# Performance work log

Hardware: AMD Instinct MI355X
Metric: run time of the kernel (lower is better)

## Reference

```python
import jax, jax.numpy as jnp
import numpy as np

N_NODES = 20000; N_EDGES = 200000
FN = 128; FE = 64; D = 128; T = 128; K = 5
H = 4; DH = D // H; N_LAYERS = 2; FF = 4 * D
B = 32768
T0 = 0.0; EPS = 1e-5


def _ln(x, s, b):
    m = jnp.mean(x, axis=-1, keepdims=True)
    v = jnp.mean(jnp.square(x - m), axis=-1, keepdims=True)
    return (x - m) / jnp.sqrt(v + EPS) * s + b


def setup_inputs() -> dict:
    key = jax.random.key(0)
    ks = jax.random.split(key, 24)
    def w(i, shape, s=0.05):
        return jax.random.normal(ks[i], shape, jnp.float32) * s
    return {
        "src": jax.random.randint(ks[0], (B,), 0, N_NODES),
        "dst": jax.random.randint(ks[1], (B,), 0, N_NODES),
        "neg": jax.random.randint(ks[2], (B,), 0, N_NODES),
        "eidx": jax.random.randint(ks[3], (B,), 0, N_EDGES),
        "ts": jax.random.uniform(ks[4], (B,), jnp.float32) * 1000.0,
        "node_feats": w(5, (N_NODES, FN), 1.0),
        "edge_feats": w(6, (N_EDGES, FE), 1.0),
        "node_lin_w": w(7, (D, FN)), "node_lin_b": jnp.zeros((D,), jnp.float32),
        "edge_lin_w": w(8, (D, FE)), "edge_lin_b": jnp.zeros((D,), jnp.float32),
        "time_w": w(9, (T,), 1.0), "time_b": w(10, (T,), 1.0),
        "tok_w": w(11, (D, 3 * D + T)), "tok_b": jnp.zeros((D,), jnp.float32),
        "qkv_w": w(12, (N_LAYERS, 3 * D, D)), "qkv_b": jnp.zeros((N_LAYERS, 3 * D), jnp.float32),
        "attn_w": w(13, (N_LAYERS, D, D)), "attn_b": jnp.zeros((N_LAYERS, D), jnp.float32),
        "ln1_s": jnp.ones((N_LAYERS, D), jnp.float32), "ln1_b": jnp.zeros((N_LAYERS, D), jnp.float32),
        "ln2_s": jnp.ones((N_LAYERS, D), jnp.float32), "ln2_b": jnp.zeros((N_LAYERS, D), jnp.float32),
        "ff1_w": w(14, (N_LAYERS, FF, D)), "ff1_b": jnp.zeros((N_LAYERS, FF), jnp.float32),
        "ff2_w": w(15, (N_LAYERS, D, FF)), "ff2_b": jnp.zeros((N_LAYERS, D), jnp.float32),
        "p1_w": w(16, (D, D)), "p1_b": jnp.zeros((D,), jnp.float32),
        "p2_w": w(17, (K, D)), "p2_b": jnp.zeros((K,), jnp.float32),
    }


def reference(src, dst, neg, eidx, ts, node_feats, edge_feats,
              node_lin_w, node_lin_b, edge_lin_w, edge_lin_b,
              time_w, time_b, tok_w, tok_b,
              qkv_w, qkv_b, attn_w, attn_b,
              ln1_s, ln1_b, ln2_s, ln2_b,
              ff1_w, ff1_b, ff2_w, ff2_b,
              p1_w, p1_b, p2_w, p2_b):
    # --- occurrence tokens: [src occs | dst occs | neg occs] = 3B tokens ---
    self_nodes = jnp.concatenate([src, dst, neg])          # [3B]
    other_nodes = jnp.concatenate([dst, src, src])         # [3B]
    eidx_all = jnp.concatenate([eidx, eidx, eidx])
    ts_all = jnp.concatenate([ts, ts, ts])
    Ntot = self_nodes.shape[0]

    base_self = node_feats[self_nodes] @ node_lin_w.T + node_lin_b    # [3B, D]
    base_other = node_feats[other_nodes] @ node_lin_w.T + node_lin_b
    edge_emb = edge_feats[eidx_all] @ edge_lin_w.T + edge_lin_b       # [3B, D]
    time_emb = jnp.cos((ts_all - T0)[:, None] * time_w[None, :] + time_b)  # [3B, T]
    x_cat = jnp.concatenate([base_self, base_other, edge_emb, time_emb], axis=-1)
    tok = jax.nn.relu(x_cat @ tok_w.T + tok_b)                        # [3B, D]

    # --- group occurrences by node, sort by time, pad (device-side) ---
    node_ids = jnp.unique(self_nodes)                      # [Nn]
    order = jnp.lexsort((ts_all, self_nodes))              # primary node, secondary time
    nodes_s = self_nodes[order]
    row_s = jnp.searchsorted(node_ids, nodes_s)            # row per sorted occ
    starts = jnp.searchsorted(nodes_s, node_ids)           # start of each group
    pos_s = jnp.arange(Ntot) - starts[row_s]               # pos within group
    node_row = jnp.zeros((Ntot,), jnp.int32).at[order].set(row_s.astype(jnp.int32))
    pos_map = jnp.zeros((Ntot,), jnp.int32).at[order].set(pos_s.astype(jnp.int32))
    seq_len = jnp.diff(jnp.concatenate([starts, jnp.array([Ntot], starts.dtype)]))
    Nn = int(node_ids.shape[0])
    Lmax = int(seq_len.max())

    x_pad = jnp.zeros((Nn, Lmax, D), tok.dtype).at[node_row, pos_map].set(tok)
    pad_mask = jnp.arange(Lmax)[None, :] >= seq_len[:, None]  # True = padded key

    # --- pre-LN TransformerEncoder (gelu, no final norm) ---
    scale = jnp.float32(1.0 / np.sqrt(DH))
    x = x_pad
    for l in range(N_LAYERS):
        h = _ln(x, ln1_s[l], ln1_b[l])
        qkv = h @ qkv_w[l].T + qkv_b[l]                    # [Nn, L, 3D]
        q, k, v = jnp.split(qkv, 3, axis=-1)
        q = q.reshape(Nn, Lmax, H, DH); k = k.reshape(Nn, Lmax, H, DH); v = v.reshape(Nn, Lmax, H, DH)
        scores = jnp.einsum('nqhd,nkhd->nhqk', q, k) * scale
        scores = jnp.where(pad_mask[:, None, None, :], jnp.float32(-1e9), scores)
        a = jax.nn.softmax(scores, axis=-1)
        o = jnp.einsum('nhqk,nkhd->nqhd', a, v).reshape(Nn, Lmax, D)
        x = x + o @ attn_w[l].T + attn_b[l]
        h2 = _ln(x, ln2_s[l], ln2_b[l])
        x = x + jax.nn.gelu(h2 @ ff1_w[l].T + ff1_b[l], approximate=False) @ ff2_w[l].T + ff2_b[l]

    # --- gather per-occurrence outputs and project to community probs ---
    def proj(hh):
        return jax.nn.softmax(jax.nn.relu(hh @ p1_w.T + p1_b) @ p2_w.T + p2_b, axis=-1)
    src_h = x[node_row[:B], pos_map[:B]]
    dst_h = x[node_row[B:2 * B], pos_map[B:2 * B]]
    neg_h = x[node_row[2 * B:], pos_map[2 * B:]]
    return proj(src_h), proj(dst_h), proj(neg_h)
```

## Files before the change

### kernel.cpp

```cpp
#include <hip/hip_runtime.h>
#include <hip/hip_bf16.h>
#include <math.h>

#define NB 32768
#define NTOK (3 * NB)
#define NNODES 20000
#define MAXL 64

typedef short bf16x8 __attribute__((ext_vector_type(8)));
typedef float f32x4 __attribute__((ext_vector_type(4)));

typedef __attribute__((address_space(3))) void lds_t;
typedef const __attribute__((address_space(1))) void gbl_t;

__device__ __forceinline__ float b2f(short s) {
    unsigned int u = ((unsigned int)(unsigned short)s) << 16;
    union { unsigned int u; float f; } c;
    c.u = u;
    return c.f;
}


__global__ void convert_k(const float* __restrict__ in, __hip_bfloat16* __restrict__ out, int n) {
    int i = blockIdx.x * 256 + threadIdx.x;
    int stride = gridDim.x * 256;
    for (; i < n; i += stride) out[i] = __float2bfloat16(in[i]);
}

__global__ void fold12_k(const float* __restrict__ tok_w, const float* __restrict__ nl_w,
                         __hip_bfloat16* __restrict__ A12) {
    int idx = blockIdx.x * 256 + threadIdx.x;
    if (idx >= 256 * 128) return;
    int n = idx >> 7, f = idx & 127;
    const float* tw = (n < 128) ? (tok_w + n * 512) : (tok_w + (n - 128) * 512 + 128);
    float acc = 0.f;
    for (int c = 0; c < 128; ++c) acc += tw[c] * nl_w[c * 128 + f];
    A12[idx] = __float2bfloat16(acc);
}

__global__ void foldE_k(const float* __restrict__ tok_w, const float* __restrict__ el_w,
                        __hip_bfloat16* __restrict__ AE) {
    int idx = blockIdx.x * 256 + threadIdx.x;
    if (idx >= 128 * 192) return;
    int d = idx / 192, j = idx % 192;
    float acc;
    if (j < 64) {
        acc = 0.f;
        for (int c = 0; c < 128; ++c) acc += tok_w[d * 512 + 256 + c] * el_w[c * 64 + j];
    } else {
        acc = tok_w[d * 512 + 384 + (j - 64)];
    }
    AE[idx] = __float2bfloat16(acc);
}

__global__ void foldb_k(const float* __restrict__ tok_w, const float* __restrict__ tok_b,
                        const float* __restrict__ nl_b, const float* __restrict__ el_b,
                        float* __restrict__ bf) {
    int d = threadIdx.x;
    if (d >= 128) return;
    float acc = tok_b[d];
    for (int c = 0; c < 128; ++c)
        acc += (tok_w[d * 512 + c] + tok_w[d * 512 + 128 + c]) * nl_b[c];
    for (int c = 0; c < 128; ++c)
        acc += tok_w[d * 512 + 256 + c] * el_b[c];
    bf[d] = acc;
}

__device__ __forceinline__ int self_node(int t, const int* src, const int* dst, const int* neg) {
    if (t < NB) return src[t];
    if (t < 2 * NB) return dst[t - NB];
    return neg[t - 2 * NB];
}

__global__ void count_k(const int* __restrict__ src, const int* __restrict__ dst,
                        const int* __restrict__ neg, int* __restrict__ cnt) {
    int t = blockIdx.x * 256 + threadIdx.x;
    if (t >= NTOK) return;
    atomicAdd(&cnt[self_node(t, src, dst, neg)], 1);
}

__global__ __launch_bounds__(1024) void scan_k(const int* __restrict__ cnt,
                                               int* __restrict__ starts) {
    __shared__ int ps[1024];
    int t = threadIdx.x;
    const int PER = 20;
    int base = t * PER;
    int loc[PER];
    int s = 0;
#pragma unroll
    for (int k = 0; k < PER; ++k) {
        int i = base + k;
        int v = (i < NNODES) ? cnt[i] : 0;
        loc[k] = s;
        s += v;
    }
    ps[t] = s;
    __syncthreads();
    for (int off = 1; off < 1024; off <<= 1) {
        int v = (t >= off) ? ps[t - off] : 0;
        __syncthreads();
        ps[t] += v;
        __syncthreads();
    }
    int offv = (t > 0) ? ps[t - 1] : 0;
#pragma unroll
    for (int k = 0; k < PER; ++k) {
        int i = base + k;
        if (i < NNODES) starts[i] = offv + loc[k];
    }
}

__global__ void scatter_k(const int* __restrict__ src, const int* __restrict__ dst,
                          const int* __restrict__ neg, const int* __restrict__ starts,
                          int* __restrict__ cursor, int* __restrict__ order) {
    int t = blockIdx.x * 256 + threadIdx.x;
    if (t >= NTOK) return;
    int node = self_node(t, src, dst, neg);
    int p = atomicAdd(&cursor[node], 1);
    order[starts[node] + p] = t;
}

__global__ void aemb_k(const int* __restrict__ eidx, const float* __restrict__ ts,
                       const float* __restrict__ ef, const float* __restrict__ tw,
                       const float* __restrict__ tb, __hip_bfloat16* __restrict__ Aemb) {
    int idx = blockIdx.x * 256 + threadIdx.x;
    if (idx >= NB * 192) return;
    int m = idx / 192, j = idx % 192;
    float v;
    if (j < 64) v = ef[(size_t)eidx[m] * 64 + j];
    else { int c = j - 64; v = cosf(ts[m] * tw[c] + tb[c]); }
    Aemb[idx] = __float2bfloat16(v);
}

__global__ __launch_bounds__(256) void asm_emb_k(
    const int* __restrict__ order, const int* __restrict__ src, const int* __restrict__ dst,
    const int* __restrict__ neg, const float* __restrict__ P12, const float* __restrict__ E,
    const float* __restrict__ s, const float* __restrict__ b,
    float* __restrict__ x, __hip_bfloat16* __restrict__ h) {
    int p = blockIdx.x * 4 + (threadIdx.x >> 6);
    int lane = threadIdx.x & 63;
    int t = order[p];
    int m, self, other;
    if (t < NB) { m = t; self = src[m]; other = dst[m]; }
    else if (t < 2 * NB) { m = t - NB; self = dst[m]; other = src[m]; }
    else { m = t - 2 * NB; self = neg[m]; other = src[m]; }
    int d0 = lane, d1 = lane + 64;
    float v0 = P12[(size_t)self * 256 + d0] + P12[(size_t)other * 256 + 128 + d0] +
               E[(size_t)m * 128 + d0];
    float v1 = P12[(size_t)self * 256 + d1] + P12[(size_t)other * 256 + 128 + d1] +
               E[(size_t)m * 128 + d1];
    v0 = fmaxf(v0, 0.f);
    v1 = fmaxf(v1, 0.f);
    float sum = v0 + v1;
#pragma unroll
    for (int off = 32; off; off >>= 1) sum += __shfl_xor(sum, off, 64);
    float mean = sum * (1.f / 128.f);
    float c0 = v0 - mean, c1 = v1 - mean;
    float vs = c0 * c0 + c1 * c1;
#pragma unroll
    for (int off = 32; off; off >>= 1) vs += __shfl_xor(vs, off, 64);
    float inv = rsqrtf(vs * (1.f / 128.f) + 1e-5f);
    x[(size_t)p * 128 + d0] = v0;
    x[(size_t)p * 128 + d1] = v1;
    h[(size_t)p * 128 + d0] = __float2bfloat16(c0 * inv * s[d0] + b[d0]);
    h[(size_t)p * 128 + d1] = __float2bfloat16(c1 * inv * s[d1] + b[d1]);
}

__device__ __forceinline__ float gelu_f(float v) {
    float ax = fabsf(v) * 0.70710678118654752f;
    float t = 1.f / (1.f + 0.3275911f * ax);
    float poly = ((((1.061405429f * t - 1.453152027f) * t + 1.421413741f) * t -
                   0.284496736f) * t + 0.254829592f) * t;
    float erf_ax = 1.f - poly * __expf(-ax * ax);
    float erfv = (v < 0.f) ? -erf_ax : erf_ax;
    return 0.5f * v * (1.f + erfv);
}

#define G_F32 0
#define G_BF16 1
#define G_GELU 2
#define G_ADD_LN 3
#define G_ADD_BF16 4

template <int MODE>
__global__ __launch_bounds__(256, 4) void gemm5_k(
    const __hip_bfloat16* __restrict__ A, const __hip_bfloat16* __restrict__ B,
    const float* __restrict__ bias, float* __restrict__ x,
    const float* __restrict__ lns, const float* __restrict__ lnb,
    __hip_bfloat16* __restrict__ hout, float* __restrict__ Cf, int N, int K) {
    __shared__ __align__(16) __hip_bfloat16 sA[2][128 * 32];
    __shared__ __align__(16) __hip_bfloat16 sB[2][128 * 32];
    __shared__ float redS[2][128];
    __shared__ float redS2[2][128];
    int tid = threadIdx.x;
    int lane = tid & 63, wid = tid >> 6;
    int wm = wid & 1, wn = wid >> 1;
    int mBase = blockIdx.x * 128, nBase = blockIdx.y * 128;
    f32x4 acc[4][4];
#pragma unroll
    for (int i = 0; i < 4; ++i)
#pragma unroll
        for (int j = 0; j < 4; ++j) {
            f32x4 z = {0.f, 0.f, 0.f, 0.f};
            acc[i][j] = z;
        }

    auto stage = [&](int buf, int k0) {
#pragma unroll
        for (int i = 0; i < 2; ++i) {
            int cid = i * 256 + tid;
            int row = cid >> 2, slotS = cid & 3;
            int slotG = slotS ^ (row & 3);
            const __hip_bfloat16* ga = A + (size_t)(mBase + row) * K + k0 + slotG * 8;
            const __hip_bfloat16* gb = B + (size_t)(nBase + row) * K + k0 + slotG * 8;
            __builtin_amdgcn_global_load_lds((gbl_t*)ga, (lds_t*)&sA[buf][(cid & ~63) * 8],
                                             16, 0, 0);
            __builtin_amdgcn_global_load_lds((gbl_t*)gb, (lds_t*)&sB[buf][(cid & ~63) * 8],
                                             16, 0, 0);
        }
    };

    int nt = K >> 5;
    stage(0, 0);
    int cur = 0;
    for (int t = 0; t < nt; ++t) {
        if (t + 1 < nt) {
            stage(cur ^ 1, (t + 1) << 5);
            asm volatile("s_waitcnt vmcnt(4)" ::: "memory");
        } else {
            asm volatile("s_waitcnt vmcnt(0)" ::: "memory");
        }
        __builtin_amdgcn_s_barrier();
        __builtin_amdgcn_sched_barrier(0);
        const bf16x8* AsV = reinterpret_cast<const bf16x8*>(sA[cur]);
        const bf16x8* BsV = reinterpret_cast<const bf16x8*>(sB[cur]);
        bf16x8 a[4], b[4];
        int kvec = lane >> 4;
#pragma unroll
        for (int f = 0; f < 4; ++f) {
            int ra = wm * 64 + f * 16 + (lane & 15);
            a[f] = AsV[ra * 4 + (kvec ^ (ra & 3))];
            int rb = wn * 64 + f * 16 + (lane & 15);
            b[f] = BsV[rb * 4 + (kvec ^ (rb & 3))];
        }
        __builtin_amdgcn_s_setprio(1);
#pragma unroll
        for (int fm = 0; fm < 4; ++fm)
#pragma unroll
            for (int fn = 0; fn < 4; ++fn)
                acc[fm][fn] = __builtin_amdgcn_mfma_f32_16x16x32_bf16(
                    a[fm], b[fn], acc[fm][fn], 0, 0, 0);
        __builtin_amdgcn_s_setprio(0);
        __builtin_amdgcn_s_barrier();
        cur ^= 1;
    }

    if (MODE == G_F32 || MODE == G_BF16 || MODE == G_GELU) {
        int colBase = nBase + wn * 64;
#pragma unroll
        for (int fm = 0; fm < 4; ++fm) {
            int row0 = mBase + wm * 64 + fm * 16 + (lane >> 4) * 4;
#pragma unroll
            for (int fn = 0; fn < 4; ++fn) {
                int col = colBase + fn * 16 + (lane & 15);
                float bv = bias ? bias[col] : 0.f;
#pragma unroll
                for (int j = 0; j < 4; ++j) {
                    float v = acc[fm][fn][j] + bv;
                    if (MODE == G_F32) {
                        Cf[(size_t)(row0 + j) * N + col] = v;
                    } else if (MODE == G_GELU) {
                        hout[(size_t)(row0 + j) * N + col] = __float2bfloat16(gelu_f(v));
                    } else {
                        hout[(size_t)(row0 + j) * N + col] = __float2bfloat16(v);
                    }
                }
            }
        }
    } else {
#pragma unroll
        for (int fm = 0; fm < 4; ++fm) {
            int rl0 = wm * 64 + fm * 16 + (lane >> 4) * 4;
#pragma unroll
            for (int fn = 0; fn < 4; ++fn) {
                int col = wn * 64 + fn * 16 + (lane & 15);
                float bv = bias[col];
#pragma unroll
                for (int j = 0; j < 4; ++j) {
                    size_t off = (size_t)(mBase + rl0 + j) * 128 + col;
                    float v = acc[fm][fn][j] + bv + x[off];
                    x[off] = v;
                    acc[fm][fn][j] = v;
                }
            }
        }
        if (MODE == G_ADD_BF16) {
#pragma unroll
            for (int fm = 0; fm < 4; ++fm) {
                int rl0 = wm * 64 + fm * 16 + (lane >> 4) * 4;
#pragma unroll
                for (int fn = 0; fn < 4; ++fn) {
                    int col = wn * 64 + fn * 16 + (lane & 15);
#pragma unroll
                    for (int j = 0; j < 4; ++j)
                        hout[(size_t)(mBase + rl0 + j) * 128 + col] =
                            __float2bfloat16(acc[fm][fn][j]);
                }
            }
        } else {
#pragma unroll
            for (int fm = 0; fm < 4; ++fm) {
#pragma unroll
                for (int j = 0; j < 4; ++j) {
                    float s1 = 0.f, s2 = 0.f;
#pragma unroll
                    for (int fn = 0; fn < 4; ++fn) {
                        float v = acc[fm][fn][j];
                        s1 += v;
                        s2 += v * v;
                    }
#pragma unroll
                    for (int off = 1; off < 16; off <<= 1) {
                        s1 += __shfl_xor(s1, off, 64);
                        s2 += __shfl_xor(s2, off, 64);
                    }
                    if ((lane & 15) == 0) {
                        int rl = wm * 64 + fm * 16 + (lane >> 4) * 4 + j;
                        redS[wn][rl] = s1;
                        redS2[wn][rl] = s2;
                    }
                }
            }
            __syncthreads();
#pragma unroll
            for (int fm = 0; fm < 4; ++fm) {
                int rl0 = wm * 64 + fm * 16 + (lane >> 4) * 4;
#pragma unroll
                for (int j = 0; j < 4; ++j) {
                    int rl = rl0 + j;
                    float mean = (redS[0][rl] + redS[1][rl]) * (1.f / 128.f);
                    float var = (redS2[0][rl] + redS2[1][rl]) * (1.f / 128.f) - mean * mean;
                    float inv = rsqrtf(var + 1e-5f);
#pragma unroll
                    for (int fn = 0; fn < 4; ++fn) {
                        int col = wn * 64 + fn * 16 + (lane & 15);
                        float c = (acc[fm][fn][j] - mean) * inv;
                        hout[(size_t)(mBase + rl) * 128 + col] =
                            __float2bfloat16(c * lns[col] + lnb[col]);
                    }
                }
            }
        }
    }
}

__global__ __launch_bounds__(256) void attn_k(
    const __hip_bfloat16* __restrict__ qkv, const int* __restrict__ starts,
    const int* __restrict__ cnt, __hip_bfloat16* __restrict__ o) {
    __shared__ float sc[4][4][4][MAXL];
    int wid = threadIdx.x >> 6, lane = threadIdx.x & 63;
    int node = blockIdx.x * 4 + wid;
    if (node >= NNODES) return;
    int st = starts[node];
    int len = cnt[node];
    if (len <= 0) return;
    if (len > MAXL) len = MAXL;
    int qs = lane >> 4, li = lane & 15, h = li >> 2;
    const float scale = 0.17677669529663687f;

    for (int qb = 0; qb < len; qb += 4) {
        int qi = qb + qs;
        bool act = qi < len;
        int qidx = act ? qi : len - 1;
        bf16x8 qv = *reinterpret_cast<const bf16x8*>(
            qkv + (size_t)(st + qidx) * 384 + li * 8);
        float qf[8];
#pragma unroll
        for (int e = 0; e < 8; ++e) qf[e] = b2f(qv[e]);
        for (int j = 0; j < len; ++j) {
            bf16x8 kv = *reinterpret_cast<const bf16x8*>(
                qkv + (size_t)(st + j) * 384 + 128 + li * 8);
            float d = 0.f;
#pragma unroll
            for (int e = 0; e < 8; ++e) d += qf[e] * b2f(kv[e]);
            d += __shfl_xor(d, 1, 64);
            d += __shfl_xor(d, 2, 64);
            if ((li & 3) == 0) sc[wid][qs][h][j] = d * scale;
        }
        float mx = -1e30f;
        for (int j = li & 3; j < len; j += 4) mx = fmaxf(mx, sc[wid][qs][h][j]);
        mx = fmaxf(mx, __shfl_xor(mx, 1, 64));
        mx = fmaxf(mx, __shfl_xor(mx, 2, 64));
        float ssum = 0.f;
        for (int j = li & 3; j < len; j += 4) {
            float e = __expf(sc[wid][qs][h][j] - mx);
            sc[wid][qs][h][j] = e;
            ssum += e;
        }
        ssum += __shfl_xor(ssum, 1, 64);
        ssum += __shfl_xor(ssum, 2, 64);
        float sinv = 1.f / ssum;
        float accv[8] = {0.f, 0.f, 0.f, 0.f, 0.f, 0.f, 0.f, 0.f};
        for (int j = 0; j < len; ++j) {
            float p = sc[wid][qs][h][j];
            bf16x8 vv = *reinterpret_cast<const bf16x8*>(
                qkv + (size_t)(st + j) * 384 + 256 + li * 8);
#pragma unroll
            for (int e = 0; e < 8; ++e) accv[e] += p * b2f(vv[e]);
        }
        if (act) {
            bf16x8 ov;
#pragma unroll
            for (int e = 0; e < 8; ++e) {
                __hip_bfloat16 t = __float2bfloat16(accv[e] * sinv);
                ov[e] = *reinterpret_cast<short*>(&t);
            }
            *reinterpret_cast<bf16x8*>(o + (size_t)(st + qi) * 128 + li * 8) = ov;
        }
    }
}

__global__ __launch_bounds__(256) void p1head_k(
    const __hip_bfloat16* __restrict__ A, const __hip_bfloat16* __restrict__ B,
    const float* __restrict__ bias, const float* __restrict__ p2w,
    const float* __restrict__ p2b, const int* __restrict__ order,
    float* __restrict__ out) {
    __shared__ __align__(16) char smem[65536];
    __shared__ float p2s[640];
    __shared__ float p2bs[5];
    float4* As4 = (float4*)smem;
    float4* Bs4 = (float4*)(smem + 16384);
    float* rowbuf = (float*)smem;
    int tid = threadIdx.x;
    for (int i = tid; i < 640; i += 256) p2s[i] = p2w[i];
    if (tid < 5) p2bs[tid] = p2b[tid];
    int lane = tid & 63, wid = tid >> 6;
    int wm = wid & 1, wn = wid >> 1;
    int mBase = blockIdx.x * 128;
    f32x4 acc[4][4];
#pragma unroll
    for (int i = 0; i < 4; ++i)
#pragma unroll
        for (int j = 0; j < 4; ++j) {
            f32x4 z = {0.f, 0.f, 0.f, 0.f};
            acc[i][j] = z;
        }
    bf16x8* AsV = reinterpret_cast<bf16x8*>(As4);
    bf16x8* BsV = reinterpret_cast<bf16x8*>(Bs4);
    for (int k0 = 0; k0 < 128; k0 += 64) {
#pragma unroll
        for (int i = 0; i < 4; ++i) {
            int cid = i * 256 + tid;
            int r = cid >> 3, c = cid & 7;
            int sidx = r * 8 + (c ^ (r & 7));
            As4[sidx] = *reinterpret_cast<const float4*>(A + (size_t)(mBase + r) * 128 + k0 + c * 8);
            Bs4[sidx] = *reinterpret_cast<const float4*>(B + (size_t)r * 128 + k0 + c * 8);
        }
        __syncthreads();
#pragma unroll
        for (int kk = 0; kk < 2; ++kk) {
            bf16x8 a[4], bb[4];
            int ccol = kk * 4 + (lane >> 4);
#pragma unroll
            for (int f = 0; f < 4; ++f) {
                int ra = wm * 64 + f * 16 + (lane & 15);
                a[f] = AsV[ra * 8 + (ccol ^ (ra & 7))];
                int rb = wn * 64 + f * 16 + (lane & 15);
                bb[f] = BsV[rb * 8 + (ccol ^ (rb & 7))];
            }
#pragma unroll
            for (int fm = 0; fm < 4; ++fm)
#pragma unroll
                for (int fn = 0; fn < 4; ++fn)
                    acc[fm][fn] = __builtin_amdgcn_mfma_f32_16x16x32_bf16(
                        a[fm], bb[fn], acc[fm][fn], 0, 0, 0);
        }
        __syncthreads();
    }
#pragma unroll
    for (int fm = 0; fm < 4; ++fm) {
        int rl0 = wm * 64 + fm * 16 + (lane >> 4) * 4;
#pragma unroll
        for (int fn = 0; fn < 4; ++fn) {
            int col = wn * 64 + fn * 16 + (lane & 15);
            float bv = bias[col];
#pragma unroll
            for (int j = 0; j < 4; ++j) {
                int rl = rl0 + j;
                rowbuf[rl * 128 + (col ^ ((rl & 7) << 2))] = fmaxf(acc[fm][fn][j] + bv, 0.f);
            }
        }
    }
    __syncthreads();
    int row = tid >> 1, half = tid & 1;
    int swz = (row & 7) << 2;
    float lg[5] = {0.f, 0.f, 0.f, 0.f, 0.f};
    for (int i = 0; i < 64; ++i) {
        int col = half * 64 + i;
        float rv = rowbuf[row * 128 + (col ^ swz)];
#pragma unroll
        for (int k = 0; k < 5; ++k) lg[k] += rv * p2s[k * 128 + col];
    }
#pragma unroll
    for (int k = 0; k < 5; ++k) lg[k] += __shfl_xor(lg[k], 1, 64);
    if (half == 0) {
        float mx = -1e30f;
#pragma unroll
        for (int k = 0; k < 5; ++k) {
            lg[k] += p2bs[k];
            mx = fmaxf(mx, lg[k]);
        }
        float e[5], ssum = 0.f;
#pragma unroll
        for (int k = 0; k < 5; ++k) {
            e[k] = __expf(lg[k] - mx);
            ssum += e[k];
        }
        float si = 1.f / ssum;
        int t = order[mBase + row];
#pragma unroll
        for (int k = 0; k < 5; ++k) out[(size_t)t * 5 + k] = e[k] * si;
    }
}


extern "C" void kernel_launch(void* const* d_in, const int* in_sizes, int n_in,
                              void* d_out, int out_size, void* d_ws, size_t ws_size,
                              hipStream_t stream) {
    const int* src = (const int*)d_in[0];
    const int* dst = (const int*)d_in[1];
    const int* neg = (const int*)d_in[2];
    const int* eidx = (const int*)d_in[3];
    const float* ts = (const float*)d_in[4];
    const float* node_feats = (const float*)d_in[5];
    const float* edge_feats = (const float*)d_in[6];
    const float* node_lin_w = (const float*)d_in[7];
    const float* node_lin_b = (const float*)d_in[8];
    const float* edge_lin_w = (const float*)d_in[9];
    const float* edge_lin_b = (const float*)d_in[10];
    const float* time_w = (const float*)d_in[11];
    const float* time_b = (const float*)d_in[12];
    const float* tok_w = (const float*)d_in[13];
    const float* tok_b = (const float*)d_in[14];
    const float* qkv_w = (const float*)d_in[15];
    const float* qkv_b = (const float*)d_in[16];
    const float* attn_w = (const float*)d_in[17];
    const float* attn_b = (const float*)d_in[18];
    const float* ln1_s = (const float*)d_in[19];
    const float* ln1_b = (const float*)d_in[20];
    const float* ln2_s = (const float*)d_in[21];
    const float* ln2_b = (const float*)d_in[22];
    const float* ff1_w = (const float*)d_in[23];
    const float* ff1_b = (const float*)d_in[24];
    const float* ff2_w = (const float*)d_in[25];
    const float* ff2_b = (const float*)d_in[26];
    const float* p1_w = (const float*)d_in[27];
    const float* p1_b = (const float*)d_in[28];
    const float* p2_w = (const float*)d_in[29];
    const float* p2_b = (const float*)d_in[30];
    float* out = (float*)d_out;

    char* w = (char*)d_ws;
    auto alloc = [&](size_t bytes) {
        char* p = w;
        w += (bytes + 255) & ~(size_t)255;
        return p;
    };
    float* x = (float*)alloc((size_t)NTOK * 128 * 4);
    __hip_bfloat16* h = (__hip_bfloat16*)alloc((size_t)NTOK * 128 * 2);
    char* big = alloc((size_t)(NTOK + 64) * 512 * 2);
    __hip_bfloat16* qkvb = (__hip_bfloat16*)big;
    __hip_bfloat16* ob = (__hip_bfloat16*)(big + (size_t)(NTOK + 64) * 384 * 2);
    __hip_bfloat16* ub = (__hip_bfloat16*)big;
    float* P12 = (float*)alloc((size_t)(NNODES + 96) * 256 * 4);
    float* E = (float*)alloc((size_t)NB * 128 * 4);
    __hip_bfloat16* Aemb = (__hip_bfloat16*)alloc((size_t)NB * 192 * 2);
    __hip_bfloat16* nfb = (__hip_bfloat16*)alloc((size_t)(NNODES + 96) * 128 * 2);
    __hip_bfloat16* A12 = (__hip_bfloat16*)alloc(256 * 128 * 2);
    __hip_bfloat16* AE = (__hip_bfloat16*)alloc(128 * 192 * 2);
    float* bfold = (float*)alloc(128 * 4);
    __hip_bfloat16* qkvwb = (__hip_bfloat16*)alloc(2 * 384 * 128 * 2);
    __hip_bfloat16* attnwb = (__hip_bfloat16*)alloc(2 * 128 * 128 * 2);
    __hip_bfloat16* ff1wb = (__hip_bfloat16*)alloc(2 * 512 * 128 * 2);
    __hip_bfloat16* ff2wb = (__hip_bfloat16*)alloc(2 * 128 * 512 * 2);
    __hip_bfloat16* p1wb = (__hip_bfloat16*)alloc(128 * 128 * 2);
    int* cnt = (int*)alloc(NNODES * 4);
    int* starts = (int*)alloc(NNODES * 4);
    int* cursor = (int*)alloc(NNODES * 4);
    int* order = (int*)alloc(NTOK * 4);

    hipMemsetAsync(cnt, 0, NNODES * 4, stream);
    hipMemsetAsync(cursor, 0, NNODES * 4, stream);

    auto cvt = [&](const float* in, __hip_bfloat16* outp, int n) {
        int blocks = (n + 255) / 256;
        if (blocks > 2048) blocks = 2048;
        convert_k<<<blocks, 256, 0, stream>>>(in, outp, n);
    };
    cvt(node_feats, nfb, NNODES * 128);
    cvt(qkv_w, qkvwb, 2 * 384 * 128);
    cvt(attn_w, attnwb, 2 * 128 * 128);
    cvt(ff1_w, ff1wb, 2 * 512 * 128);
    cvt(ff2_w, ff2wb, 2 * 128 * 512);
    cvt(p1_w, p1wb, 128 * 128);

    fold12_k<<<128, 256, 0, stream>>>(tok_w, node_lin_w, A12);
    foldE_k<<<96, 256, 0, stream>>>(tok_w, edge_lin_w, AE);
    foldb_k<<<1, 128, 0, stream>>>(tok_w, tok_b, node_lin_b, edge_lin_b, bfold);

    count_k<<<(NTOK + 255) / 256, 256, 0, stream>>>(src, dst, neg, cnt);
    scan_k<<<1, 1024, 0, stream>>>(cnt, starts);
    scatter_k<<<(NTOK + 255) / 256, 256, 0, stream>>>(src, dst, neg, starts, cursor, order);

    aemb_k<<<(NB * 192 + 255) / 256, 256, 0, stream>>>(eidx, ts, edge_feats, time_w, time_b, Aemb);

    gemm5_k<G_F32><<<dim3(157, 2), 256, 0, stream>>>(
        nfb, A12, nullptr, nullptr, nullptr, nullptr, nullptr, P12, 256, 128);
    gemm5_k<G_F32><<<dim3(256, 1), 256, 0, stream>>>(
        Aemb, AE, bfold, nullptr, nullptr, nullptr, nullptr, E, 128, 192);
    asm_emb_k<<<NTOK / 4, 256, 0, stream>>>(order, src, dst, neg, P12, E,
                                            ln1_s, ln1_b, x, h);

    const int gm = NTOK / 128;
    for (int l = 0; l < 2; ++l) {
        gemm5_k<G_BF16><<<dim3(gm, 3), 256, 0, stream>>>(
            h, qkvwb + (size_t)l * 384 * 128, qkv_b + l * 384,
            nullptr, nullptr, nullptr, qkvb, nullptr, 384, 128);
        attn_k<<<(NNODES + 3) / 4, 256, 0, stream>>>(qkvb, starts, cnt, ob);
        gemm5_k<G_ADD_LN><<<dim3(gm, 1), 256, 0, stream>>>(
            ob, attnwb + (size_t)l * 128 * 128, attn_b + l * 128,
            x, ln2_s + l * 128, ln2_b + l * 128, h, nullptr, 128, 128);
        gemm5_k<G_GELU><<<dim3(gm, 4), 256, 0, stream>>>(
            h, ff1wb + (size_t)l * 512 * 128, ff1_b + l * 512,
            nullptr, nullptr, nullptr, ub, nullptr, 512, 128);
        if (l == 0)
            gemm5_k<G_ADD_LN><<<dim3(gm, 1), 256, 0, stream>>>(
                ub, ff2wb, ff2_b, x, ln1_s + 128, ln1_b + 128, h, nullptr, 128, 512);
        else
            gemm5_k<G_ADD_BF16><<<dim3(gm, 1), 256, 0, stream>>>(
                ub, ff2wb + (size_t)128 * 512, ff2_b + 128, x,
                nullptr, nullptr, h, nullptr, 128, 512);
    }

    p1head_k<<<gm, 256, 0, stream>>>(h, p1wb, p1_b, p2_w, p2_b, order, out);
}
```

Measured before the change: 604.1 us.

## Add weight-resident persistent GEMM kernel with vectorized epilogues for K≤192 GEMMs

Adds gemm6_k, which loads the full 128-column weight tile for the whole K dimension into LDS once. It then loops persistently over M tiles, double-buffering only the activation tile and prefetching the next tile's first chunk. The MFMA operands are swapped so each lane holds 4 consecutive columns, which allows float4 and bf16x4 vector stores and float4 bias and LN-parameter loads in the epilogue. The LDS swizzle in gemm5_k is strengthened to reduce bank conflicts. The trade-off is more LDS per block (lower occupancy, launch bounds 3) and fixed persistent grid sizes in exchange for removing repeated weight reloads and scalar stores.

```diff
diff --git a/kernel.cpp b/kernel.cpp
--- a/kernel.cpp
+++ b/kernel.cpp
@@ -8,6 +8,7 @@
 #define MAXL 64
 
 typedef short bf16x8 __attribute__((ext_vector_type(8)));
+typedef short bf16x4 __attribute__((ext_vector_type(4)));
 typedef float f32x4 __attribute__((ext_vector_type(4)));
 
 typedef __attribute__((address_space(3))) void lds_t;
@@ -18,6 +19,16 @@
     union { unsigned int u; float f; } c;
     c.u = u;
     return c.f;
+}
+
+__device__ __forceinline__ void store4(__hip_bfloat16* p, float a, float b, float c, float d) {
+    bf16x4 o;
+    __hip_bfloat16 t;
+    t = __float2bfloat16(a); o[0] = *reinterpret_cast<short*>(&t);
+    t = __float2bfloat16(b); o[1] = *reinterpret_cast<short*>(&t);
+    t = __float2bfloat16(c); o[2] = *reinterpret_cast<short*>(&t);
+    t = __float2bfloat16(d); o[3] = *reinterpret_cast<short*>(&t);
+    *reinterpret_cast<bf16x4*>(p) = o;
 }
 
 
@@ -182,6 +193,179 @@
 #define G_ADD_LN 3
 #define G_ADD_BF16 4
 
+template <int MODE, int KK>
+__global__ __launch_bounds__(256, 3) void gemm6_k(
+    const __hip_bfloat16* __restrict__ A, const __hip_bfloat16* __restrict__ B,
+    const float* __restrict__ bias, float* __restrict__ x,
+    const float* __restrict__ lns, const float* __restrict__ lnb,
+    __hip_bfloat16* __restrict__ hout, float* __restrict__ Cf,
+    int N, int numM) {
+    constexpr int CH = KK / 32;
+    constexpr int BSLOT = KK / 8;
+    __shared__ __align__(16) __hip_bfloat16 sB[128 * KK];
+    __shared__ __align__(16) __hip_bfloat16 sA[2][128 * 32];
+    int tid = threadIdx.x;
+    int lane = tid & 63, wid = tid >> 6;
+    int li = lane & 15, lq = lane >> 4;
+    int nBase = blockIdx.y * 128;
+
+#pragma unroll
+    for (int i = 0; i < KK / 16; ++i) {
+        int cid = i * 256 + tid;
+        int row = cid / BSLOT, slotS = cid % BSLOT;
+        int slotG = slotS ^ (row & 7);
+        const __hip_bfloat16* gb = B + (size_t)(nBase + row) * KK + slotG * 8;
+        __builtin_amdgcn_global_load_lds((gbl_t*)gb, (lds_t*)&sB[(cid & ~63) * 8], 16, 0, 0);
+    }
+    auto stageA = [&](int buf, int mi, int c) {
+#pragma unroll
+        for (int i = 0; i < 2; ++i) {
+            int cid = i * 256 + tid;
+            int row = cid >> 2, slotS = cid & 3;
+            int slotG = slotS ^ ((row & 3) ^ ((row >> 2) & 3));
+            const __hip_bfloat16* ga =
+                A + (size_t)(mi * 128 + row) * KK + c * 32 + slotG * 8;
+            __builtin_amdgcn_global_load_lds((gbl_t*)ga, (lds_t*)&sA[buf][(cid & ~63) * 8],
+                                             16, 0, 0);
+        }
+    };
+
+    int mi = blockIdx.x;
+    if (mi < numM) stageA(0, mi, 0);
+    const bf16x8* BsV = reinterpret_cast<const bf16x8*>(sB);
+
+    while (mi < numM) {
+        int nextMi = mi + gridDim.x;
+        f32x4 acc[2][8];
+#pragma unroll
+        for (int i = 0; i < 2; ++i)
+#pragma unroll
+            for (int j = 0; j < 8; ++j) {
+                f32x4 z = {0.f, 0.f, 0.f, 0.f};
+                acc[i][j] = z;
+            }
+        for (int c = 0; c < CH; ++c) {
+            if (c + 1 < CH) {
+                stageA((c + 1) & 1, mi, c + 1);
+                asm volatile("s_waitcnt vmcnt(2)" ::: "memory");
+            } else if (nextMi < numM) {
+                stageA(0, nextMi, 0);
+                asm volatile("s_waitcnt vmcnt(2)" ::: "memory");
+            } else {
+                asm volatile("s_waitcnt vmcnt(0)" ::: "memory");
+            }
+            __builtin_amdgcn_s_barrier();
+            __builtin_amdgcn_sched_barrier(0);
+            const bf16x8* AsV = reinterpret_cast<const bf16x8*>(sA[c & 1]);
+            bf16x8 a[2], b[8];
+#pragma unroll
+            for (int fm = 0; fm < 2; ++fm) {
+                int ra = wid * 32 + fm * 16 + li;
+                a[fm] = AsV[ra * 4 + (lq ^ ((ra & 3) ^ ((ra >> 2) & 3)))];
+            }
+            int kvb = c * 4 + lq;
+#pragma unroll
+            for (int fn = 0; fn < 8; ++fn) {
+                int rb = fn * 16 + li;
+                b[fn] = BsV[rb * BSLOT + (kvb ^ (rb & 7))];
+            }
+            __builtin_amdgcn_s_setprio(1);
+#pragma unroll
+            for (int fm = 0; fm < 2; ++fm)
+#pragma unroll
+                for (int fn = 0; fn < 8; ++fn)
+                    acc[fm][fn] = __builtin_amdgcn_mfma_f32_16x16x32_bf16(
+                        b[fn], a[fm], acc[fm][fn], 0, 0, 0);
+            __builtin_amdgcn_s_setprio(0);
+            __builtin_amdgcn_s_barrier();
+        }
+        int rowG0 = mi * 128 + wid * 32;
+        if (MODE == G_F32 || MODE == G_BF16 || MODE == G_GELU) {
+#pragma unroll
+            for (int fm = 0; fm < 2; ++fm) {
+                int row = rowG0 + fm * 16 + li;
+#pragma unroll
+                for (int fn = 0; fn < 8; ++fn) {
+                    int col = nBase + fn * 16 + lq * 4;
+                    float4 bv = {0.f, 0.f, 0.f, 0.f};
+                    if (bias) bv = *reinterpret_cast<const float4*>(bias + col);
+                    f32x4 v = acc[fm][fn];
+                    float v0 = v[0] + bv.x, v1 = v[1] + bv.y;
+                    float v2 = v[2] + bv.z, v3 = v[3] + bv.w;
+                    if (MODE == G_GELU) {
+                        v0 = gelu_f(v0); v1 = gelu_f(v1); v2 = gelu_f(v2); v3 = gelu_f(v3);
+                    }
+                    if (MODE == G_F32) {
+                        float4 o = {v0, v1, v2, v3};
+                        *reinterpret_cast<float4*>(Cf + (size_t)row * N + col) = o;
+                    } else {
+                        store4(hout + (size_t)row * N + col, v0, v1, v2, v3);
+                    }
+                }
+            }
+        } else {
+            float s1[2] = {0.f, 0.f}, s2[2] = {0.f, 0.f};
+#pragma unroll
+            for (int fm = 0; fm < 2; ++fm) {
+                int row = rowG0 + fm * 16 + li;
+#pragma unroll
+                for (int fn = 0; fn < 8; ++fn) {
+                    int col = fn * 16 + lq * 4;
+                    float4 bv = *reinterpret_cast<const float4*>(bias + col);
+                    float4 xv = *reinterpret_cast<float4*>(x + (size_t)row * 128 + col);
+                    f32x4 v = acc[fm][fn];
+                    v[0] += bv.x + xv.x; v[1] += bv.y + xv.y;
+                    v[2] += bv.z + xv.z; v[3] += bv.w + xv.w;
+                    acc[fm][fn] = v;
+                    float4 o = {v[0], v[1], v[2], v[3]};
+                    *reinterpret_cast<float4*>(x + (size_t)row * 128 + col) = o;
+                    s1[fm] += v[0] + v[1] + v[2] + v[3];
+                    s2[fm] += v[0] * v[0] + v[1] * v[1] + v[2] * v[2] + v[3] * v[3];
+                }
+            }
+            if (MODE == G_ADD_BF16) {
+#pragma unroll
+                for (int fm = 0; fm < 2; ++fm) {
+                    int row = rowG0 + fm * 16 + li;
+#pragma unroll
+                    for (int fn = 0; fn < 8; ++fn) {
+                        int col = fn * 16 + lq * 4;
+                        f32x4 v = acc[fm][fn];
+                        store4(hout + (size_t)row * 128 + col, v[0], v[1], v[2], v[3]);
+                    }
+                }
+            } else {
+#pragma unroll
+                for (int fm = 0; fm < 2; ++fm) {
+                    float a1 = s1[fm];
+                    a1 += __shfl_xor(a1, 16, 64);
+                    a1 += __shfl_xor(a1, 32, 64);
+                    float a2 = s2[fm];
+                    a2 += __shfl_xor(a2, 16, 64);
+                    a2 += __shfl_xor(a2, 32, 64);
+                    float mean = a1 * (1.f / 128.f);
+                    float var = a2 * (1.f / 128.f) - mean * mean;
+                    float inv = rsqrtf(var + 1e-5f);
+                    int row = rowG0 + fm * 16 + li;
+#pragma unroll
+                    for (int fn = 0; fn < 8; ++fn) {
+                        int col = fn * 16 + lq * 4;
+                        float4 sv = *reinterpret_cast<const float4*>(lns + col);
+                        float4 bv2 = *reinterpret_cast<const float4*>(lnb + col);
+                        f32x4 v = acc[fm][fn];
+                        store4(hout + (size_t)row * 128 + col,
+                               (v[0] - mean) * inv * sv.x + bv2.x,
+                               (v[1] - mean) * inv * sv.y + bv2.y,
+                               (v[2] - mean) * inv * sv.z + bv2.z,
+                               (v[3] - mean) * inv * sv.w + bv2.w);
+                    }
+                }
+            }
+        }
+        mi = nextMi;
+    }
+}
+
 template <int MODE>
 __global__ __launch_bounds__(256, 4) void gemm5_k(
     const __hip_bfloat16* __restrict__ A, const __hip_bfloat16* __restrict__ B,
@@ -210,7 +394,7 @@
         for (int i = 0; i < 2; ++i) {
             int cid = i * 256 + tid;
             int row = cid >> 2, slotS = cid & 3;
-            int slotG = slotS ^ (row & 3);
+            int slotG = slotS ^ ((row & 3) ^ ((row >> 2) & 3));
             const __hip_bfloat16* ga = A + (size_t)(mBase + row) * K + k0 + slotG * 8;
             const __hip_bfloat16* gb = B + (size_t)(nBase + row) * K + k0 + slotG * 8;
             __builtin_amdgcn_global_load_lds((gbl_t*)ga, (lds_t*)&sA[buf][(cid & ~63) * 8],
@@ -239,9 +423,9 @@
 #pragma unroll
         for (int f = 0; f < 4; ++f) {
             int ra = wm * 64 + f * 16 + (lane & 15);
-            a[f] = AsV[ra * 4 + (kvec ^ (ra & 3))];
+            a[f] = AsV[ra * 4 + (kvec ^ ((ra & 3) ^ ((ra >> 2) & 3)))];
             int rb = wn * 64 + f * 16 + (lane & 15);
-            b[f] = BsV[rb * 4 + (kvec ^ (rb & 3))];
+            b[f] = BsV[rb * 4 + (kvec ^ ((rb & 3) ^ ((rb >> 2) & 3)))];
         }
         __builtin_amdgcn_s_setprio(1);
 #pragma unroll
@@ -255,99 +439,75 @@
         cur ^= 1;
     }
 
-    if (MODE == G_F32 || MODE == G_BF16 || MODE == G_GELU) {
-        int colBase = nBase + wn * 64;
-#pragma unroll
-        for (int fm = 0; fm < 4; ++fm) {
-            int row0 = mBase + wm * 64 + fm * 16 + (lane >> 4) * 4;
-#pragma unroll
-            for (int fn = 0; fn < 4; ++fn) {
-                int col = colBase + fn * 16 + (lane & 15);
-                float bv = bias ? bias[col] : 0.f;
-#pragma unroll
-                for (int j = 0; j < 4; ++j) {
-                    float v = acc[fm][fn][j] + bv;
-                    if (MODE == G_F32) {
-                        Cf[(size_t)(row0 + j) * N + col] = v;
-                    } else if (MODE == G_GELU) {
-                        hout[(size_t)(row0 + j) * N + col] = __float2bfloat16(gelu_f(v));
-                    } else {
-                        hout[(size_t)(row0 + j) * N + col] = __float2bfloat16(v);
-                    }
-                }
-            }
-        }
-    } else {
+#pragma unroll
+    for (int fm = 0; fm < 4; ++fm) {
+        int rl0 = wm * 64 + fm * 16 + (lane >> 4) * 4;
+#pragma unroll
+        for (int fn = 0; fn < 4; ++fn) {
+            int col = wn * 64 + fn * 16 + (lane & 15);
+            float bv = bias[col];
+#pragma unroll
+            for (int j = 0; j < 4; ++j) {
+                size_t off = (size_t)(mBase + rl0 + j) * 128 + col;
+                float v = acc[fm][fn][j] + bv + x[off];
+                x[off] = v;
+                acc[fm][fn][j] = v;
+            }
+        }
+    }
+    if (MODE == G_ADD_BF16) {
 #pragma unroll
         for (int fm = 0; fm < 4; ++fm) {
             int rl0 = wm * 64 + fm * 16 + (lane >> 4) * 4;
 #pragma unroll
             for (int fn = 0; fn < 4; ++fn) {
                 int col = wn * 64 + fn * 16 + (lane & 15);
-                float bv = bias[col];
-#pragma unroll
-                for (int j = 0; j < 4; ++j) {
-                    size_t off = (size_t)(mBase + rl0 + j) * 128 + col;
-                    float v = acc[fm][fn][j] + bv + x[off];
-                    x[off] = v;
-                    acc[fm][fn][j] = v;
+#pragma unroll
+                for (int j = 0; j < 4; ++j)
+                    hout[(size_t)(mBase + rl0 + j) * 128 + col] =
+                        __float2bfloat16(acc[fm][fn][j]);
+            }
+        }
+    } else {
+#pragma unroll
+        for (int fm = 0; fm < 4; ++fm) {
+#pragma unroll
+            for (int j = 0; j < 4; ++j) {
+                float s1 = 0.f, s2 = 0.f;
+#pragma unroll
+                for (int fn = 0; fn < 4; ++fn) {
+                    float v = acc[fm][fn][j];
+                    s1 += v;
+                    s2 += v * v;
                 }
-            }
-        }
-        if (MODE == G_ADD_BF16) {
-#pragma unroll
-            for (int fm = 0; fm < 4; ++fm) {
-                int rl0 = wm * 64 + fm * 16 + (lane >> 4) * 4;
+#pragma unroll
+                for (int off = 1; off < 16; off <<= 1) {
+                    s1 += __shfl_xor(s1, off, 64);
+                    s2 += __shfl_xor(s2, off, 64);
+                }
+                if ((lane & 15) == 0) {
+                    int rl = wm * 64 + fm * 16 + (lane >> 4) * 4 + j;
+                    redS[wn][rl] = s1;
+                    redS2[wn][rl] = s2;
+                }
+            }
+        }
+        __syncthreads();
+#pragma unroll
+        for (int fm = 0; fm < 4; ++fm) {
+            int rl0 = wm * 64 + fm * 16 + (lane >> 4) * 4;
+#pragma unroll
+            for (int j = 0; j < 4; ++j) {
+                int rl = rl0 + j;
+                float mean = (redS[0][rl] + redS[1][rl]) * (1.f / 128.f);
+                float var = (redS2[0][rl] + redS2[1][rl]) * (1.f / 128.f) - mean * mean;
+                float inv = rsqrtf(var + 1e-5f);
 #pragma unroll
                 for (int fn = 0; fn < 4; ++fn) {
                     int col = wn * 64 + fn * 16 + (lane & 15);
-#pragma unroll
-                    for (int j = 0; j < 4; ++j)
-                        hout[(size_t)(mBase + rl0 + j) * 128 + col] =
-                            __float2bfloat16(acc[fm][fn][j]);
-                }
-            }
-        } else {
-#pragma unroll
-            for (int fm = 0; fm < 4; ++fm) {
-#pragma unroll
-                for (int j = 0; j < 4; ++j) {
-                    float s1 = 0.f, s2 = 0.f;
-#pragma unroll
-                    for (int fn = 0; fn < 4; ++fn) {
-                        float v = acc[fm][fn][j];
-                        s1 += v;
-                        s2 += v * v;
-                    }
-#pragma unroll
-                    for (int off = 1; off < 16; off <<= 1) {
-                        s1 += __shfl_xor(s1, off, 64);
-                        s2 += __shfl_xor(s2, off, 64);
-                    }
-                    if ((lane & 15) == 0) {
-                        int rl = wm * 64 + fm * 16 + (lane >> 4) * 4 + j;
-                        redS[wn][rl] = s1;
-                        redS2[wn][rl] = s2;
-                    }
-                }
-            }
-            __syncthreads();
-#pragma unroll
-            for (int fm = 0; fm < 4; ++fm) {
-                int rl0 = wm * 64 + fm * 16 + (lane >> 4) * 4;
-#pragma unroll
-                for (int j = 0; j < 4; ++j) {
-                    int rl = rl0 + j;
-                    float mean = (redS[0][rl] + redS[1][rl]) * (1.f / 128.f);
-                    float var = (redS2[0][rl] + redS2[1][rl]) * (1.f / 128.f) - mean * mean;
-                    float inv = rsqrtf(var + 1e-5f);
-#pragma unroll
-                    for (int fn = 0; fn < 4; ++fn) {
-                        int col = wn * 64 + fn * 16 + (lane & 15);
-                        float c = (acc[fm][fn][j] - mean) * inv;
-                        hout[(size_t)(mBase + rl) * 128 + col] =
-                            __float2bfloat16(c * lns[col] + lnb[col]);
-                    }
+                    float c = (acc[fm][fn][j] - mean) * inv;
+                    hout[(size_t)(mBase + rl) * 128 + col] =
+                        __float2bfloat16(c * lns[col] + lnb[col]);
                 }
             }
         }
@@ -614,25 +774,25 @@
 
     aemb_k<<<(NB * 192 + 255) / 256, 256, 0, stream>>>(eidx, ts, edge_feats, time_w, time_b, Aemb);
 
-    gemm5_k<G_F32><<<dim3(157, 2), 256, 0, stream>>>(
-        nfb, A12, nullptr, nullptr, nullptr, nullptr, nullptr, P12, 256, 128);
-    gemm5_k<G_F32><<<dim3(256, 1), 256, 0, stream>>>(
-        Aemb, AE, bfold, nullptr, nullptr, nullptr, nullptr, E, 128, 192);
+    gemm6_k<G_F32, 128><<<dim3(157, 2), 256, 0, stream>>>(
+        nfb, A12, nullptr, nullptr, nullptr, nullptr, nullptr, P12, 256, 157);
+    gemm6_k<G_F32, 192><<<dim3(256, 1), 256, 0, stream>>>(
+        Aemb, AE, bfold, nullptr, nullptr, nullptr, nullptr, E, 128, 256);
     asm_emb_k<<<NTOK / 4, 256, 0, stream>>>(order, src, dst, neg, P12, E,
                                             ln1_s, ln1_b, x, h);
 
     const int gm = NTOK / 128;
     for (int l = 0; l < 2; ++l) {
-        gemm5_k<G_BF16><<<dim3(gm, 3), 256, 0, stream>>>(
+        gemm6_k<G_BF16, 128><<<dim3(256, 3), 256, 0, stream>>>(
             h, qkvwb + (size_t)l * 384 * 128, qkv_b + l * 384,
-            nullptr, nullptr, nullptr, qkvb, nullptr, 384, 128);
+            nullptr, nullptr, nullptr, qkvb, nullptr, 384, gm);
         attn_k<<<(NNODES + 3) / 4, 256, 0, stream>>>(qkvb, starts, cnt, ob);
-        gemm5_k<G_ADD_LN><<<dim3(gm, 1), 256, 0, stream>>>(
+        gemm6_k<G_ADD_LN, 128><<<dim3(gm, 1), 256, 0, stream>>>(
             ob, attnwb + (size_t)l * 128 * 128, attn_b + l * 128,
-            x, ln2_s + l * 128, ln2_b + l * 128, h, nullptr, 128, 128);
-        gemm5_k<G_GELU><<<dim3(gm, 4), 256, 0, stream>>>(
+            x, ln2_s + l * 128, ln2_b + l * 128, h, nullptr, 128, gm);
+        gemm6_k<G_GELU, 128><<<dim3(192, 4), 256, 0, stream>>>(
             h, ff1wb + (size_t)l * 512 * 128, ff1_b + l * 512,
-            nullptr, nullptr, nullptr, ub, nullptr, 512, 128);
+            nullptr, nullptr, nullptr, ub, nullptr, 512, gm);
         if (l == 0)
             gemm5_k<G_ADD_LN><<<dim3(gm, 1), 256, 0, stream>>>(
                 ub, ff2wb, ff2_b, x, ln1_s + 128, ln1_b + 128, h, nullptr, 128, 512);
```

Measured after the change: 646.6 us. 7.0% more time.
